# Kernel tuning notes

Measured on AMD Instinct MI355X. Metric: run time of the kernel, lower is better.

Reference implementation:

```python
import jax, jax.numpy as jnp
import numpy as np

N, G, K = 16384, 32, 8          # cells, hvg genes (32*32 covet), n_neighs
IN_DIM, HID, OUT = 2000, 1024, 30


def setup_inputs() -> dict:
    key = jax.random.key(0)
    ks = jax.random.split(key, 8)
    return {
        "x": jax.random.normal(ks[0], (N, IN_DIM), jnp.float32),
        "coordinates": jax.random.uniform(ks[1], (N, 2), jnp.float32) * 100.0,
        "highly_variable_genes": jax.random.uniform(ks[2], (N, G), jnp.float32),
        # fc1: Linear(input_dim + 32*32, hidden); stored as [in, out]
        "W1": jax.random.normal(ks[3], (IN_DIM + G * G, HID), jnp.float32) * 0.02,
        "b1": jnp.zeros((HID,), jnp.float32),
        "W2": jax.random.normal(ks[4], (HID, OUT), jnp.float32) * 0.02,
        "b2": jnp.zeros((OUT,), jnp.float32),
    }


def _covet_sqrt(genes, coords, k):
    # brute-force kNN over spatial coordinates (squared euclidean)
    sq = jnp.sum(coords * coords, axis=1)                      # [N]
    d2 = sq[:, None] + sq[None, :] - 2.0 * (coords @ coords.T)  # [N, N]
    _, idx = jax.lax.top_k(-d2, k)                             # [N, k] nearest (incl. self)
    neigh = genes[idx]                                         # [N, k, G] irregular gather
    # COVET: center neighborhoods at the GLOBAL mean expression
    centered = neigh - jnp.mean(genes, axis=0)                 # [N, k, G]
    cov = jnp.einsum('nkg,nkh->ngh', centered, centered) / (k - 1)  # [N, G, G]
    # matrix square root of each PSD covariance via eigh
    w, V = jnp.linalg.eigh(cov)
    s = jnp.sqrt(jnp.clip(w, 0.0, None))                       # [N, G]
    return jnp.einsum('ngk,nk,nhk->ngh', V, s, V)              # V diag(s) V^T


def reference(x, coordinates, highly_variable_genes, W1, b1, W2, b2):
    # original runs covet_sqrt in numpy -> detached from autograd
    covet = jax.lax.stop_gradient(
        _covet_sqrt(highly_variable_genes, coordinates, K))
    hidden = jnp.concatenate([x, covet.reshape(-1, G * G)], axis=1)  # [N, IN+1024]
    h = jax.nn.relu(hidden @ W1 + b1)
    return h @ W2 + b2
```

## Files before the change

### kernel.cpp

```cpp
#include <hip/hip_runtime.h>
#include <hip/hip_bf16.h>
#include <math.h>

#define N_CELLS 16384
#define G_GENES 32
#define IN_DIM  2000
#define HID     1024
#define OUT_DIM 30
#define K_TOT   3024
#define K_PAD   3040
#define NT      95
#define GRID_B  128
#define NBINS   (GRID_B * GRID_B)
#define SCELL   (100.0f / (float)GRID_B)
#define CSCALE  0.37796447300922722721f

typedef unsigned short ushort_t;
typedef __attribute__((ext_vector_type(8))) short bf16x8;
typedef __attribute__((ext_vector_type(4))) short bf16x4;
typedef __attribute__((ext_vector_type(4))) float f32x4;

__device__ __forceinline__ ushort_t f2bf(float v) {
  return __builtin_bit_cast(ushort_t, __float2bfloat16(v));
}

__device__ __forceinline__ void glds16(const void* g, void* l) {
  __builtin_amdgcn_global_load_lds(
      (const __attribute__((address_space(1))) unsigned int*)g,
      (__attribute__((address_space(3))) unsigned int*)l, 16, 0, 0);
}

__global__ __launch_bounds__(256) void fused_pre(const float* __restrict__ x,
                                                 const float* __restrict__ W1,
                                                 const float* __restrict__ W2,
                                                 const float* __restrict__ genes,
                                                 const float* __restrict__ coords,
                                                 ushort_t* __restrict__ Abf,
                                                 ushort_t* __restrict__ Bh,
                                                 ushort_t* __restrict__ W2t,
                                                 double* __restrict__ part,
                                                 int* __restrict__ cnt,
                                                 int* __restrict__ binOf) {
  __shared__ float L[32][260];
  __shared__ double red[256];
  const int bid = blockIdx.x;
  const int tid = threadIdx.x;

  if (bid < 380) {
    const int cb = bid / NT, t = bid % NT;
    const int k0 = t * 32, n0 = cb * 256;
    {
      const int kl = tid >> 3;
      const int nw = tid & 7;
#pragma unroll
      for (int u = 0; u < 8; ++u) {
        const int nl = (nw + u * 8) * 4;
        float4 v = make_float4(0.f, 0.f, 0.f, 0.f);
        if (k0 + kl < K_TOT) v = *(const float4*)(W1 + (size_t)(k0 + kl) * HID + n0 + nl);
        L[kl][nl + 0] = v.x; L[kl][nl + 1] = v.y; L[kl][nl + 2] = v.z; L[kl][nl + 3] = v.w;
      }
    }
    __syncthreads();
    const size_t tileBase = ((size_t)cb * NT + t) * 8192;
    const int n = tid;
#pragma unroll
    for (int q = 0; q < 4; ++q) {
      const int cdata = q ^ ((n >> 1) & 3);
      ushort_t hi[8];
#pragma unroll
      for (int e = 0; e < 8; ++e) {
        const int kl = cdata * 8 + e;
        const float v = (k0 + kl < K_TOT) ? L[kl][n] : 0.f;
        hi[e] = f2bf(v);
      }
      *(bf16x8*)(Bh + tileBase + ((size_t)n * 4 + q) * 8) = *(const bf16x8*)hi;
    }
  } else if (bid < 384) {
    const int k = (bid - 380) * 256 + tid;
#pragma unroll
    for (int o = 0; o < 32; ++o) {
      const float v = (o < OUT_DIM) ? W2[k * OUT_DIM + o] : 0.f;
      W2t[o * HID + k] = f2bf(v);
    }
  } else if (bid < 2432) {
    const int rbase = (bid - 384) * 8;
#pragma unroll
    for (int rr = 0; rr < 8; ++rr) {
      const int row = rbase + rr;
      if (tid < 250) {
#pragma unroll
        for (int ph = 0; ph < 2; ++ph) {
          const int col = ph * 1000 + tid * 4;
          const float4 v = *(const float4*)(x + (size_t)row * IN_DIM + col);
          ushort_t o[4] = { f2bf(v.x), f2bf(v.y), f2bf(v.z), f2bf(v.w) };
          *(bf16x4*)(Abf + (size_t)row * K_PAD + col) = *(const bf16x4*)o;
        }
      } else if (tid < 252) {
        const bf16x8 z = (bf16x8){0, 0, 0, 0, 0, 0, 0, 0};
        *(bf16x8*)(Abf + (size_t)row * K_PAD + K_TOT + (tid - 250) * 8) = z;
      }
    }
  } else if (bid < 2560) {
    const int b = bid - 2432;
    const int g = tid & 31, cs = tid >> 5;
    double acc = 0.0;
#pragma unroll
    for (int it = 0; it < 16; ++it) {
      const int cell = b * 128 + cs + it * 8;
      acc += (double)genes[cell * G_GENES + g];
    }
    red[tid] = acc;
    __syncthreads();
    if (tid < 32) {
      double s = red[tid];
#pragma unroll
      for (int u = 1; u < 8; ++u) s += red[tid + u * 32];
      part[b * 32 + tid] = s;
    }
  } else {
    const int i = (bid - 2560) * 256 + tid;
    const float2 p = ((const float2*)coords)[i];
    const float inv_s = (float)GRID_B / 100.0f;
    const int bx = min(GRID_B - 1, max(0, (int)(p.x * inv_s)));
    const int by = min(GRID_B - 1, max(0, (int)(p.y * inv_s)));
    const int b = by * GRID_B + bx;
    binOf[i] = b;
    atomicAdd(&cnt[b], 1);
  }
}

__global__ __launch_bounds__(256) void scan_fin(const int* __restrict__ cnt,
                                                int* __restrict__ binStart,
                                                int* __restrict__ cursor,
                                                const double* __restrict__ part,
                                                float* __restrict__ meanv) {
  const int tid = threadIdx.x;
  if (blockIdx.x == 0) {
    __shared__ int ps[256];
    int s = 0;
    for (int i = 0; i < 64; ++i) s += cnt[tid * 64 + i];
    ps[tid] = s;
    __syncthreads();
    for (int off = 1; off < 256; off <<= 1) {
      const int add = (tid >= off) ? ps[tid - off] : 0;
      __syncthreads();
      ps[tid] += add;
      __syncthreads();
    }
    int run = ps[tid] - s;
    for (int i = 0; i < 64; ++i) {
      const int b = tid * 64 + i;
      binStart[b] = run;
      cursor[b] = run;
      run += cnt[b];
    }
    if (tid == 255) binStart[NBINS] = run;
  } else {
    if (tid < 32) {
      double s = 0.0;
      for (int b = 0; b < 128; ++b) s += part[b * 32 + tid];
      meanv[tid] = (float)(s / (double)N_CELLS);
    }
  }
}

__global__ __launch_bounds__(256) void bin_scatter(const float* __restrict__ coords,
                                                   const int* __restrict__ binOf,
                                                   int* __restrict__ cursor,
                                                   int* __restrict__ binPts,
                                                   float2* __restrict__ sxy) {
  const int i = blockIdx.x * 256 + threadIdx.x;
  const float2 p = ((const float2*)coords)[i];
  const int pos = atomicAdd(&cursor[binOf[i]], 1);
  binPts[pos] = i;
  sxy[pos] = p;
}

__global__ __launch_bounds__(64) void knn_search(const int* __restrict__ binStart,
                                                 const int* __restrict__ binPts,
                                                 const float2* __restrict__ sxy,
                                                 int* __restrict__ nidx) {
  const int rank = blockIdx.x * 64 + threadIdx.x;
  const int cell = binPts[rank];
  const float2 qv = sxy[rank];
  const float qx = qv.x, qy = qv.y;
  const float sqi = __fadd_rn(__fmul_rn(qx, qx), __fmul_rn(qy, qy));
  const float inv_s = (float)GRID_B / 100.0f;
  const int bx = min(GRID_B - 1, max(0, (int)(qx * inv_s)));
  const int by = min(GRID_B - 1, max(0, (int)(qy * inv_s)));

  unsigned long long kk[8];
#pragma unroll
  for (int i = 0; i < 8; ++i) kk[i] = ~0ull;

  auto scan_seg = [&](int s, int e) {
    for (int p = s; p < e; ++p) {
      const float2 pc = sxy[p];
      const int j = binPts[p];
      const float sqj = __fadd_rn(__fmul_rn(pc.x, pc.x), __fmul_rn(pc.y, pc.y));
      const float dot = __fmaf_rn(qy, pc.y, __fmul_rn(qx, pc.x));
      const float d2  = __fsub_rn(__fadd_rn(sqi, sqj), __fmul_rn(2.0f, dot));
      unsigned int sb = __float_as_uint(d2);
      sb = (sb & 0x80000000u) ? ~sb : (sb | 0x80000000u);
      unsigned long long key = ((unsigned long long)sb << 32) | (unsigned int)j;
      if (key < kk[7]) {
#pragma unroll
        for (int q2 = 0; q2 < 8; ++q2) {
          const bool lt = key < kk[q2];
          const unsigned long long tmp = kk[q2];
          kk[q2] = lt ? key : kk[q2];
          key = lt ? tmp : key;
        }
      }
    }
  };

  bool done = false;
  for (int r = 0; r < GRID_B; ++r) {
    if (!done) {
      if (r == 0) {
        const int b = by * GRID_B + bx;
        scan_seg(binStart[b], binStart[b + 1]);
      } else {
        const int xlo = max(0, bx - r), xhi = min(GRID_B - 1, bx + r);
        if (by - r >= 0) {
          const int b0 = (by - r) * GRID_B;
          scan_seg(binStart[b0 + xlo], binStart[b0 + xhi + 1]);
        }
        if (by + r < GRID_B) {
          const int b0 = (by + r) * GRID_B;
          scan_seg(binStart[b0 + xlo], binStart[b0 + xhi + 1]);
        }
        for (int dy = -r + 1; dy <= r - 1; ++dy) {
          const int yy = by + dy;
          if (yy < 0 || yy >= GRID_B) continue;
          if (bx - r >= 0) { const int b = yy * GRID_B + bx - r; scan_seg(binStart[b], binStart[b + 1]); }
          if (bx + r < GRID_B) { const int b = yy * GRID_B + bx + r; scan_seg(binStart[b], binStart[b + 1]); }
        }
      }
      if (kk[7] != ~0ull) {
        const unsigned int sb = (unsigned int)(kk[7] >> 32);
        const float wd2 = __uint_as_float((sb & 0x80000000u) ? (sb ^ 0x80000000u) : ~sb);
        const float bnd = (float)r * SCELL;
        if (wd2 < bnd * bnd * 0.998f - 0.05f) done = true;
      }
    }
    if (!__any(!done)) break;
  }
#pragma unroll
  for (int i = 0; i < 8; ++i) nidx[cell * 8 + i] = (int)(kk[i] & 0xFFFFFFFFu);
}

__global__ __launch_bounds__(256) void gram_kernel(const float* __restrict__ genes,
                                                   const float* __restrict__ meanv,
                                                   const int* __restrict__ nidx,
                                                   float* __restrict__ GwsT) {
  const int wv = threadIdx.x >> 6, lane = threadIdx.x & 63;
  const int bidl = (blockIdx.x & 7) * 512 + (blockIdx.x >> 3);
  const int cell = bidl * 4 + wv;
  __shared__ float A[4][8][36];
  {
    const int n = lane >> 3;
    const int c = (lane & 7) << 2;
    const int src = nidx[cell * 8 + n];
    const float4 v = *(const float4*)(genes + (size_t)src * G_GENES + c);
    float o[4] = { (v.x - meanv[c + 0]) * CSCALE, (v.y - meanv[c + 1]) * CSCALE,
                   (v.z - meanv[c + 2]) * CSCALE, (v.w - meanv[c + 3]) * CSCALE };
    *(float4*)&A[wv][n][c] = *(const float4*)o;
  }
  __syncthreads();
  const int i = lane >> 3, j = lane & 7;
  float acc = 0.f;
#pragma unroll
  for (int g = 0; g < 32; ++g) acc = fmaf(A[wv][i][g], A[wv][j][g], acc);
  GwsT[(size_t)lane * N_CELLS + cell] = acc;
}

__global__ __launch_bounds__(64) void jacobi_kernel(const float* __restrict__ GwsT,
                                                    float* __restrict__ VwsT,
                                                    float* __restrict__ lamT) {
  const int cell = blockIdx.x * 64 + threadIdx.x;
  float Gm[8][8], V[8][8];
#pragma unroll
  for (int e = 0; e < 64; ++e) Gm[e >> 3][e & 7] = GwsT[(size_t)e * N_CELLS + cell];
#pragma unroll
  for (int i = 0; i < 8; ++i)
#pragma unroll
    for (int j = 0; j < 8; ++j) V[i][j] = (i == j) ? 1.0f : 0.0f;

  for (int sweep = 0; sweep < 5; ++sweep) {
#pragma unroll
    for (int p = 0; p < 7; ++p) {
#pragma unroll
      for (int q = p + 1; q < 8; ++q) {
        const float apq = Gm[p][q];
        const float app = Gm[p][p], aqq = Gm[q][q];
        float t;
        if (apq != 0.0f) {
          const float tau = (aqq - app) * __builtin_amdgcn_rcpf(2.0f * apq);
          const float r = sqrtf(fmaf(tau, tau, 1.0f));
          t = copysignf(1.0f, tau) * __builtin_amdgcn_rcpf(fabsf(tau) + r);
        } else {
          t = 0.0f;
        }
        const float c = __builtin_amdgcn_rsqf(fmaf(t, t, 1.0f));
        const float s = t * c;
#pragma unroll
        for (int r2 = 0; r2 < 8; ++r2) {
          const float gp = Gm[p][r2], gq = Gm[q][r2];
          Gm[p][r2] = fmaf(c, gp, -s * gq);
          Gm[q][r2] = fmaf(s, gp,  c * gq);
        }
#pragma unroll
        for (int r2 = 0; r2 < 8; ++r2) {
          const float gp = Gm[r2][p], gq = Gm[r2][q];
          Gm[r2][p] = fmaf(c, gp, -s * gq);
          Gm[r2][q] = fmaf(s, gp,  c * gq);
        }
#pragma unroll
        for (int r2 = 0; r2 < 8; ++r2) {
          const float vp = V[r2][p], vq = V[r2][q];
          V[r2][p] = fmaf(c, vp, -s * vq);
          V[r2][q] = fmaf(s, vp,  c * vq);
        }
      }
    }
  }
#pragma unroll
  for (int e = 0; e < 64; ++e) VwsT[(size_t)e * N_CELLS + cell] = V[e >> 3][e & 7];
#pragma unroll
  for (int m = 0; m < 8; ++m) lamT[(size_t)m * N_CELLS + cell] = Gm[m][m];
}

__global__ __launch_bounds__(256) void recon_kernel(const float* __restrict__ genes,
                                                    const float* __restrict__ meanv,
                                                    const int* __restrict__ nidx,
                                                    const float* __restrict__ VwsT,
                                                    const float* __restrict__ lamT,
                                                    ushort_t* __restrict__ Abf) {
  const int wv = threadIdx.x >> 6, lane = threadIdx.x & 63;
  const int cell = blockIdx.x * 4 + wv;
  __shared__ float A[4][8][36];
  __shared__ float Ws[4][8][33];
  __shared__ float Vs[4][64];
  __shared__ float lamS[4][8];
  {
    const int n = lane >> 3;
    const int c = (lane & 7) << 2;
    const int src = nidx[cell * 8 + n];
    const float4 v = *(const float4*)(genes + (size_t)src * G_GENES + c);
    float o[4] = { (v.x - meanv[c + 0]) * CSCALE, (v.y - meanv[c + 1]) * CSCALE,
                   (v.z - meanv[c + 2]) * CSCALE, (v.w - meanv[c + 3]) * CSCALE };
    *(float4*)&A[wv][n][c] = *(const float4*)o;
  }
  Vs[wv][lane] = VwsT[(size_t)lane * N_CELLS + cell];
  if (lane < 8) lamS[wv][lane] = lamT[(size_t)lane * N_CELLS + cell];
  __syncthreads();

  float maxl = 0.f;
#pragma unroll
  for (int m = 0; m < 8; ++m) maxl = fmaxf(maxl, lamS[wv][m]);
  const float thr = maxl * 1e-8f;

#pragma unroll
  for (int q = 0; q < 4; ++q) {
    const int e = lane + (q << 6);
    const int m = e >> 5, g = e & 31;
    float acc = 0.f;
#pragma unroll
    for (int i = 0; i < 8; ++i) acc = fmaf(Vs[wv][i * 8 + m], A[wv][i][g], acc);
    const float l = lamS[wv][m];
    const float scm = (l > thr) ? sqrtf(1.0f / sqrtf(l)) : 0.0f;
    Ws[wv][m][g] = acc * scm;
  }
  __syncthreads();
  ushort_t* dst = Abf + (size_t)cell * K_PAD + IN_DIM;
#pragma unroll
  for (int r = 0; r < 16; ++r) {
    const int o = (r << 6) + lane;
    const int g = o >> 5, hh = o & 31;
    float acc = 0.f;
#pragma unroll
    for (int m = 0; m < 8; ++m) acc = fmaf(Ws[wv][m][g], Ws[wv][m][hh], acc);
    dst[o] = f2bf(acc);
  }
}

__global__ __launch_bounds__(512, 4) void gemm1_kernel(const ushort_t* __restrict__ Abf,
                                                       const ushort_t* __restrict__ Bh,
                                                       const float* __restrict__ b1,
                                                       ushort_t* __restrict__ h) {
  __shared__ ushort_t As[3][4096];
  __shared__ ushort_t Bs[3][8192];

  const int tid = threadIdx.x;
  const int id  = blockIdx.x;
  const int xcd = id & 7, local = id >> 3;
  const int rb  = (xcd << 4) + (local & 15);
  const int cb  = local >> 4;
  const int row0 = rb << 7, col0 = cb << 8;

  const int lane = tid & 63, wv = tid >> 6;
  const int m_base = (wv >> 2) << 6, n_base = (wv & 3) << 6;
  const int l15 = lane & 15, l4 = lane >> 4;

  const int arow = tid >> 2, acpos = tid & 3;
  const int acdata = acpos ^ ((arow >> 1) & 3);
  const ushort_t* aptr = Abf + (size_t)(row0 + arow) * K_PAD + acdata * 8;
  const ushort_t* bptr = Bh + (size_t)cb * NT * 8192 + tid * 8;

  int aoff[4], boff[4];
#pragma unroll
  for (int i = 0; i < 4; ++i) {
    const int r = m_base + i * 16 + l15;
    aoff[i] = r * 32 + (l4 ^ ((r >> 1) & 3)) * 8;
  }
#pragma unroll
  for (int j = 0; j < 4; ++j) {
    const int r = n_base + j * 16 + l15;
    boff[j] = r * 32 + (l4 ^ ((r >> 1) & 3)) * 8;
  }

  f32x4 acc[4][4];
#pragma unroll
  for (int i = 0; i < 4; ++i)
#pragma unroll
    for (int j = 0; j < 4; ++j) acc[i][j] = (f32x4){0.f, 0.f, 0.f, 0.f};

  auto prefetch = [&](int buf) {
    glds16(aptr,        &As[buf][tid * 8]);
    glds16(bptr,        &Bs[buf][tid * 8]);
    glds16(bptr + 4096, &Bs[buf][tid * 8 + 4096]);
    aptr += 32;
    bptr += 8192;
  };
  auto compute = [&](int buf) {
    bf16x8 ah[4], bh[4];
#pragma unroll
    for (int i = 0; i < 4; ++i) ah[i] = *(const bf16x8*)(&As[buf][aoff[i]]);
#pragma unroll
    for (int j = 0; j < 4; ++j) bh[j] = *(const bf16x8*)(&Bs[buf][boff[j]]);
#pragma unroll
    for (int i = 0; i < 4; ++i)
#pragma unroll
      for (int j = 0; j < 4; ++j)
        acc[i][j] = __builtin_amdgcn_mfma_f32_16x16x32_bf16(ah[i], bh[j], acc[i][j], 0, 0, 0);
  };

  prefetch(0);
  prefetch(1);
  asm volatile("s_waitcnt vmcnt(3)" ::: "memory");
  __builtin_amdgcn_s_barrier();
  __builtin_amdgcn_sched_barrier(0);

#define STEP(BUFC, BUFP) { prefetch(BUFP); compute(BUFC); \
    asm volatile("s_waitcnt vmcnt(3)" ::: "memory"); \
    __builtin_amdgcn_s_barrier(); \
    __builtin_amdgcn_sched_barrier(0); }
  for (int tt = 0; tt < 31; ++tt) {
    STEP(0, 2)
    STEP(1, 0)
    STEP(2, 1)
  }
#undef STEP
  compute(0);
  asm volatile("s_waitcnt vmcnt(0)" ::: "memory");
  __builtin_amdgcn_s_barrier();
  __builtin_amdgcn_sched_barrier(0);
  compute(1);

  float bb[4];
#pragma unroll
  for (int j = 0; j < 4; ++j) bb[j] = b1[col0 + n_base + j * 16 + l15];
#pragma unroll
  for (int i = 0; i < 4; ++i) {
    const int rbase = row0 + m_base + i * 16 + l4 * 4;
#pragma unroll
    for (int j = 0; j < 4; ++j) {
      const int c = col0 + n_base + j * 16 + l15;
#pragma unroll
      for (int q = 0; q < 4; ++q) {
        const float v = fmaxf(acc[i][j][q] + bb[j], 0.f);
        h[(size_t)(rbase + q) * HID + c] = f2bf(v);
      }
    }
  }
}

__global__ __launch_bounds__(256) void gemm2_kernel(const ushort_t* __restrict__ h,
                                                    const ushort_t* __restrict__ W2t,
                                                    const float* __restrict__ b2,
                                                    float* __restrict__ out) {
  const int tid = threadIdx.x;
  const int lane = tid & 63, wv = tid >> 6;
  const int rowt = wv & 1, colt = wv >> 1;
  const int l15 = lane & 15, l4 = lane >> 4;
  const int row0 = blockIdx.x * 32 + rowt * 16;
  const int col  = colt * 16 + l15;

  f32x4 acc = (f32x4){0.f, 0.f, 0.f, 0.f};
  const ushort_t* ha = h + (size_t)(row0 + l15) * HID + l4 * 8;
  const ushort_t* wb = W2t + (size_t)col * HID + l4 * 8;
#pragma unroll 8
  for (int k0 = 0; k0 < HID; k0 += 32) {
    const bf16x8 av = *(const bf16x8*)(ha + k0);
    const bf16x8 bv = *(const bf16x8*)(wb + k0);
    acc = __builtin_amdgcn_mfma_f32_16x16x32_bf16(av, bv, acc, 0, 0, 0);
  }
  if (col < OUT_DIM) {
    const float bias = b2[col];
#pragma unroll
    for (int q = 0; q < 4; ++q) {
      const int r = row0 + l4 * 4 + q;
      out[(size_t)r * OUT_DIM + col] = acc[q] + bias;
    }
  }
}

extern "C" void kernel_launch(void* const* d_in, const int* in_sizes, int n_in,
                              void* d_out, int out_size, void* d_ws, size_t ws_size,
                              hipStream_t stream) {
  (void)in_sizes; (void)n_in; (void)out_size;
  const float* x      = (const float*)d_in[0];
  const float* coords = (const float*)d_in[1];
  const float* genes  = (const float*)d_in[2];
  const float* W1     = (const float*)d_in[3];
  const float* b1     = (const float*)d_in[4];
  const float* W2     = (const float*)d_in[5];
  const float* b2     = (const float*)d_in[6];
  float* out = (float*)d_out;

  char* ws = (char*)d_ws;
  size_t off = 0;
  auto alloc = [&](size_t bytes) -> void* {
    void* p = ws + off;
    off = (off + bytes + 255) & ~(size_t)255;
    return p;
  };
  ushort_t* Abf    = (ushort_t*)alloc((size_t)N_CELLS * K_PAD * 2);
  ushort_t* hbf    = (ushort_t*)alloc((size_t)N_CELLS * HID * 2);
  ushort_t* Bh     = (ushort_t*)alloc((size_t)4 * NT * 8192 * 2);
  ushort_t* W2t    = (ushort_t*)alloc((size_t)32 * HID * 2);
  float*    GwsT   = (float*)alloc((size_t)64 * N_CELLS * 4);
  float*    VwsT   = (float*)alloc((size_t)64 * N_CELLS * 4);
  float*    lamT   = (float*)alloc((size_t)8 * N_CELLS * 4);
  int*      nidx   = (int*)alloc((size_t)N_CELLS * 8 * 4);
  double*   part   = (double*)alloc((size_t)128 * 32 * 8);
  float*    meanv  = (float*)alloc(G_GENES * 4);
  int*      binCnt = (int*)alloc((size_t)NBINS * 4);
  int*      binSt  = (int*)alloc((size_t)(NBINS + 1) * 4);
  int*      cursor = (int*)alloc((size_t)NBINS * 4);
  int*      binOf  = (int*)alloc((size_t)N_CELLS * 4);
  int*      binPts = (int*)alloc((size_t)N_CELLS * 4);
  float2*   sxy    = (float2*)alloc((size_t)N_CELLS * 8);
  if (off > ws_size) return;

  hipMemsetAsync(binCnt, 0, (size_t)NBINS * 4, stream);

  hipLaunchKernelGGL(fused_pre,   dim3(2624),  dim3(256), 0, stream,
                     x, W1, W2, genes, coords, Abf, Bh, W2t, part, binCnt, binOf);
  hipLaunchKernelGGL(scan_fin,    dim3(2),     dim3(256), 0, stream, binCnt, binSt, cursor, part, meanv);
  hipLaunchKernelGGL(bin_scatter, dim3(64),    dim3(256), 0, stream, coords, binOf, cursor, binPts, sxy);
  hipLaunchKernelGGL(knn_search,  dim3(256),   dim3(64),  0, stream, binSt, binPts, sxy, nidx);
  hipLaunchKernelGGL(gram_kernel, dim3(4096),  dim3(256), 0, stream, genes, meanv, nidx, GwsT);
  hipLaunchKernelGGL(jacobi_kernel, dim3(256), dim3(64),  0, stream, GwsT, VwsT, lamT);
  hipLaunchKernelGGL(recon_kernel,  dim3(4096), dim3(256), 0, stream, genes, meanv, nidx, VwsT, lamT, Abf);
  hipLaunchKernelGGL(gemm1_kernel,  dim3(512),  dim3(512), 0, stream, Abf, Bh, b1, hbf);
  hipLaunchKernelGGL(gemm2_kernel,  dim3(512),  dim3(256), 0, stream, hbf, W2t, b2, out);
}
```

Before: 266.9 us.

## Fuse second linear layer into gemm1 epilogue with split-K partial reduction

The ReLU hidden tile is now staged in shared memory instead of being written to global as bf16. Each gemm1 block multiplies its 128x256 hidden tile by the matching W2 slice with MFMA and writes per-column-block partial outputs. A small reduce kernel then sums the four partials and adds b2. This removes the 32MB hidden-activation write and re-read, at the cost of a partial-output buffer, an extra launch and some added epilogue work in gemm1.

```diff
diff --git a/kernel.cpp b/kernel.cpp
--- a/kernel.cpp
+++ b/kernel.cpp
@@ -389,9 +389,11 @@
 __global__ __launch_bounds__(512, 4) void gemm1_kernel(const ushort_t* __restrict__ Abf,
                                                        const ushort_t* __restrict__ Bh,
                                                        const float* __restrict__ b1,
-                                                       ushort_t* __restrict__ h) {
-  __shared__ ushort_t As[3][4096];
-  __shared__ ushort_t Bs[3][8192];
+                                                       const ushort_t* __restrict__ W2t,
+                                                       float* __restrict__ part4) {
+  __shared__ ushort_t smem[36864];
+  ushort_t* As = smem;
+  ushort_t* Bs = smem + 12288;
 
   const int tid = threadIdx.x;
   const int id  = blockIdx.x;
@@ -428,18 +430,18 @@
     for (int j = 0; j < 4; ++j) acc[i][j] = (f32x4){0.f, 0.f, 0.f, 0.f};
 
   auto prefetch = [&](int buf) {
-    glds16(aptr,        &As[buf][tid * 8]);
-    glds16(bptr,        &Bs[buf][tid * 8]);
-    glds16(bptr + 4096, &Bs[buf][tid * 8 + 4096]);
+    glds16(aptr,        As + buf * 4096 + tid * 8);
+    glds16(bptr,        Bs + buf * 8192 + tid * 8);
+    glds16(bptr + 4096, Bs + buf * 8192 + tid * 8 + 4096);
     aptr += 32;
     bptr += 8192;
   };
   auto compute = [&](int buf) {
     bf16x8 ah[4], bh[4];
 #pragma unroll
-    for (int i = 0; i < 4; ++i) ah[i] = *(const bf16x8*)(&As[buf][aoff[i]]);
-#pragma unroll
-    for (int j = 0; j < 4; ++j) bh[j] = *(const bf16x8*)(&Bs[buf][boff[j]]);
+    for (int i = 0; i < 4; ++i) ah[i] = *(const bf16x8*)(As + buf * 4096 + aoff[i]);
+#pragma unroll
+    for (int j = 0; j < 4; ++j) bh[j] = *(const bf16x8*)(Bs + buf * 8192 + boff[j]);
 #pragma unroll
     for (int i = 0; i < 4; ++i)
 #pragma unroll
@@ -472,49 +474,52 @@
   float bb[4];
 #pragma unroll
   for (int j = 0; j < 4; ++j) bb[j] = b1[col0 + n_base + j * 16 + l15];
+
+  __syncthreads();
+  ushort_t* Hs = smem;
 #pragma unroll
   for (int i = 0; i < 4; ++i) {
-    const int rbase = row0 + m_base + i * 16 + l4 * 4;
+    const int rl = m_base + i * 16 + l4 * 4;
 #pragma unroll
     for (int j = 0; j < 4; ++j) {
-      const int c = col0 + n_base + j * 16 + l15;
+      const int cl = n_base + j * 16 + l15;
 #pragma unroll
       for (int q = 0; q < 4; ++q) {
         const float v = fmaxf(acc[i][j][q] + bb[j], 0.f);
-        h[(size_t)(rbase + q) * HID + c] = f2bf(v);
-      }
-    }
-  }
-}
-
-__global__ __launch_bounds__(256) void gemm2_kernel(const ushort_t* __restrict__ h,
-                                                    const ushort_t* __restrict__ W2t,
-                                                    const float* __restrict__ b2,
-                                                    float* __restrict__ out) {
-  const int tid = threadIdx.x;
-  const int lane = tid & 63, wv = tid >> 6;
-  const int rowt = wv & 1, colt = wv >> 1;
-  const int l15 = lane & 15, l4 = lane >> 4;
-  const int row0 = blockIdx.x * 32 + rowt * 16;
-  const int col  = colt * 16 + l15;
-
-  f32x4 acc = (f32x4){0.f, 0.f, 0.f, 0.f};
-  const ushort_t* ha = h + (size_t)(row0 + l15) * HID + l4 * 8;
-  const ushort_t* wb = W2t + (size_t)col * HID + l4 * 8;
-#pragma unroll 8
-  for (int k0 = 0; k0 < HID; k0 += 32) {
-    const bf16x8 av = *(const bf16x8*)(ha + k0);
-    const bf16x8 bv = *(const bf16x8*)(wb + k0);
-    acc = __builtin_amdgcn_mfma_f32_16x16x32_bf16(av, bv, acc, 0, 0, 0);
-  }
-  if (col < OUT_DIM) {
-    const float bias = b2[col];
-#pragma unroll
-    for (int q = 0; q < 4; ++q) {
-      const int r = row0 + l4 * 4 + q;
-      out[(size_t)r * OUT_DIM + col] = acc[q] + bias;
-    }
-  }
+        Hs[(rl + q) * 264 + cl] = f2bf(v);
+      }
+    }
+  }
+  __syncthreads();
+
+  f32x4 o0 = (f32x4){0.f, 0.f, 0.f, 0.f};
+  f32x4 o1 = (f32x4){0.f, 0.f, 0.f, 0.f};
+  const ushort_t* w2b = W2t + col0 + l4 * 8;
+#pragma unroll
+  for (int kt = 0; kt < 8; ++kt) {
+    const bf16x8 af = *(const bf16x8*)(Hs + (wv * 16 + l15) * 264 + kt * 32 + l4 * 8);
+    const bf16x8 b0 = *(const bf16x8*)(w2b + (size_t)l15 * HID + kt * 32);
+    const bf16x8 b1f = *(const bf16x8*)(w2b + (size_t)(16 + l15) * HID + kt * 32);
+    o0 = __builtin_amdgcn_mfma_f32_16x16x32_bf16(af, b0, o0, 0, 0, 0);
+    o1 = __builtin_amdgcn_mfma_f32_16x16x32_bf16(af, b1f, o1, 0, 0, 0);
+  }
+  float* pdst = part4 + ((size_t)cb * N_CELLS + row0 + wv * 16 + l4 * 4) * 32 + l15;
+#pragma unroll
+  for (int q = 0; q < 4; ++q) {
+    pdst[q * 32]      = o0[q];
+    pdst[q * 32 + 16] = o1[q];
+  }
+}
+
+__global__ __launch_bounds__(256) void reduce_out(const float* __restrict__ part4,
+                                                  const float* __restrict__ b2,
+                                                  float* __restrict__ out) {
+  const int t = blockIdx.x * 256 + threadIdx.x;
+  const int n = t >> 5, o = t & 31;
+  if (o >= OUT_DIM) return;
+  const size_t str = (size_t)N_CELLS * 32;
+  const float s = ((part4[t] + part4[t + str]) + part4[t + 2 * str]) + part4[t + 3 * str];
+  out[(size_t)n * OUT_DIM + o] = s + b2[o];
 }
 
 extern "C" void kernel_launch(void* const* d_in, const int* in_sizes, int n_in,
@@ -538,7 +543,7 @@
     return p;
   };
   ushort_t* Abf    = (ushort_t*)alloc((size_t)N_CELLS * K_PAD * 2);
-  ushort_t* hbf    = (ushort_t*)alloc((size_t)N_CELLS * HID * 2);
+  float*    part4  = (float*)alloc((size_t)4 * N_CELLS * 32 * 4);
   ushort_t* Bh     = (ushort_t*)alloc((size_t)4 * NT * 8192 * 2);
   ushort_t* W2t    = (ushort_t*)alloc((size_t)32 * HID * 2);
   float*    GwsT   = (float*)alloc((size_t)64 * N_CELLS * 4);
@@ -565,6 +570,6 @@
   hipLaunchKernelGGL(gram_kernel, dim3(4096),  dim3(256), 0, stream, genes, meanv, nidx, GwsT);
   hipLaunchKernelGGL(jacobi_kernel, dim3(256), dim3(64),  0, stream, GwsT, VwsT, lamT);
   hipLaunchKernelGGL(recon_kernel,  dim3(4096), dim3(256), 0, stream, genes, meanv, nidx, VwsT, lamT, Abf);
-  hipLaunchKernelGGL(gemm1_kernel,  dim3(512),  dim3(512), 0, stream, Abf, Bh, b1, hbf);
-  hipLaunchKernelGGL(gemm2_kernel,  dim3(512),  dim3(256), 0, stream, hbf, W2t, b2, out);
-}
+  hipLaunchKernelGGL(gemm1_kernel,  dim3(512),  dim3(512), 0, stream, Abf, Bh, b1, W2t, part4);
+  hipLaunchKernelGGL(reduce_out,    dim3(2048), dim3(256), 0, stream, part4, b2, out);
+}
```

Result: faster. 252.4 us (-5.5%).
